# Kernel optimization log

Hardware: AMD Instinct MI355X
Metric: run time of the kernel (lower is better)

## Reference

```python
import jax, jax.numpy as jnp
import numpy as np

B, N, P, K, C = 8, 4096, 4096, 32, 128  # batch, points, npoint, neighbors, channels (=mlp[-1])
W_OUT = 16  # weightnet output channels (from Linear(16*mlp[-1], mlp[-1]))
EPS = 1e-5


def setup_inputs() -> dict:
    key = jax.random.key(0)
    ks = jax.random.split(key, 9)
    xyz = jax.random.normal(ks[0], (B, P, 3), jnp.float32)
    points = jax.random.normal(ks[1], (B, N, C), jnp.float32)
    local_coordinates = jax.random.normal(ks[2], (B, P, K, 3), jnp.float32)
    neighbor_lists = jax.random.randint(ks[3], (B, P, K), 0, N)
    data_idx = jax.random.randint(ks[4], (B,), 0, B)
    Ww = jax.random.normal(ks[5], (3, W_OUT), jnp.float32) * 0.1   # weightnet (pointwise linear 3->16)
    bw = jnp.zeros((W_OUT,), jnp.float32)
    Wl = jax.random.normal(ks[6], (W_OUT * C, C), jnp.float32) * 0.02  # nn.Linear(16*mlp[-1], mlp[-1])
    bl = jnp.zeros((C,), jnp.float32)
    gamma = jnp.ones((C,), jnp.float32)   # BatchNorm1d weight
    beta = jnp.zeros((C,), jnp.float32)   # BatchNorm1d bias
    return {"xyz": xyz, "points": points, "local_coordinates": local_coordinates,
            "neighbor_lists": neighbor_lists, "data_idx": data_idx,
            "Ww": Ww, "bw": bw, "Wl": Wl, "bl": bl, "gamma": gamma, "beta": beta}


def reference(xyz, points, local_coordinates, neighbor_lists, data_idx, Ww, bw, Wl, bl, gamma, beta):
    b, p, k, _ = local_coordinates.shape
    c = points.shape[-1]
    # weightnet: pointwise map of 3-D local coordinates to 16 weight channels -> [B,P,K,16]
    weights = local_coordinates @ Ww + bw
    # irregular neighbor gather: data[b,p,k,:] = points[b, neighbor_lists[b,p,k], :] -> [B,P,K,C]
    data = points[jnp.arange(b)[:, None, None], neighbor_lists]
    # per-point weighted aggregation over K neighbors: [B,P,C,16] -> flatten to [B,P,C*16]
    new_points = jnp.einsum('bpkc,bpkw->bpcw', data, weights).reshape(b, p, c * weights.shape[-1])
    # batch reindex via data_idx
    new_points = new_points[data_idx]
    # linear tail: [B,P,C]
    new_points = new_points @ Wl + bl
    # BatchNorm1d over channel dim (training-mode batch stats), then ReLU: [B,C,P]
    x = new_points.transpose(0, 2, 1)
    mean = x.mean(axis=(0, 2), keepdims=True)
    var = x.var(axis=(0, 2), keepdims=True)
    x = (x - mean) * jax.lax.rsqrt(var + EPS) * gamma[None, :, None] + beta[None, :, None]
    return xyz, jax.nn.relu(x)
```

## Files before the change

### kernel.cpp

```cpp
#include <hip/hip_runtime.h>

#define Bn 8
#define Nn 4096
#define Pn 4096
#define Kn 32
#define Cn 128

using float4v = __attribute__((ext_vector_type(4))) float;
using short8  = __attribute__((ext_vector_type(8))) short;

__device__ __forceinline__ unsigned short bf16b(float f) {
  union { float f; unsigned u; } v; v.f = f;
  unsigned r = v.u + 0x7FFFu + ((v.u >> 16) & 1u);
  return (unsigned short)(r >> 16);
}

__device__ __forceinline__ unsigned pkhi(float x, float y) {
  return __builtin_amdgcn_perm(__float_as_uint(y), __float_as_uint(x), 0x07060302u);
}

__global__ __launch_bounds__(256) void prep(const float* __restrict__ Wl,
                                            unsigned short* __restrict__ WlT,
                                            const float* __restrict__ xyz,
                                            float* __restrict__ out,
                                            float* __restrict__ gacc) {
  __shared__ unsigned short tile[128 * 33];
  const int t = threadIdx.x, blk = blockIdx.x;
  if (blk < 64) {
#pragma unroll
    for (int i = 0; i < 16; ++i) {
      int idx = i * 256 + t;
      int kl = idx >> 7, n = idx & 127;
      tile[n * 33 + kl] = bf16b(Wl[(size_t)(blk * 32 + kl) * 128 + n]);
    }
    __syncthreads();
#pragma unroll
    for (int i = 0; i < 16; ++i) {
      int idx = i * 256 + t;
      int n = idx >> 5, kl = idx & 31;
      WlT[(size_t)n * 2048 + blk * 32 + kl] = tile[n * 33 + kl];
    }
  } else {
    if (blk == 64) gacc[t] = 0.f;
    const int i0 = (blk - 64) * 3072 + t * 12;
#pragma unroll
    for (int i = 0; i < 3; ++i)
      *(float4v*)(out + i0 + i * 4) = *(const float4v*)(xyz + i0 + i * 4);
  }
}

__global__ __launch_bounds__(256, 4) void fused(
    const float* __restrict__ points, const float* __restrict__ lc,
    const int* __restrict__ nl, const int* __restrict__ didx,
    const float* __restrict__ Ww, const float* __restrict__ bwv,
    const unsigned short* __restrict__ WlT, const float* __restrict__ blv,
    float* __restrict__ xout, float* __restrict__ gacc) {
  __shared__ unsigned short Mlds[32 * 256 + 7424];
  __shared__ int nlds[32 * 32];
  __shared__ float red[256];

  const int t = threadIdx.x, lane = t & 63, w = t >> 6;
  const int l15 = lane & 15, q = lane >> 4;
  const int b = blockIdx.x & 7;
  const int pg = blockIdx.x >> 3;
  const int p0 = pg * 32;
  const int db = didx[b];
  const char* __restrict__ pbase = (const char*)(points + (size_t)db * Nn * Cn);

  if (blockIdx.x == 0xFFFFFFFFu) ((volatile unsigned short*)Mlds)[32 * 256 + t] = 0;

  {
    int4 nv = *(const int4*)(nl + (size_t)(db * Pn + p0) * Kn + t * 4);
    nv.x <<= 9; nv.y <<= 9; nv.z <<= 9; nv.w <<= 9;
    *(int4*)&nlds[t * 4] = nv;
  }

  const float Ww0 = Ww[l15], Ww1 = Ww[16 + l15], Ww2 = Ww[32 + l15];
  const float bw0 = bwv[l15];

  short8 af[8];
#pragma unroll
  for (int i = 0; i < 8; ++i) {
    const int p = p0 + w * 8 + i;
    const int pk = (db * Pn + p) * Kn;
    const float* __restrict__ lcp = lc + (size_t)(pk + q * 8) * 3;
    float la[24];
#pragma unroll
    for (int v = 0; v < 6; ++v) *(float4v*)&la[v * 4] = *(const float4v*)(lcp + v * 4);
#pragma unroll
    for (int j = 0; j < 8; ++j) {
      float ww = bw0 + la[3 * j] * Ww0 + la[3 * j + 1] * Ww1 + la[3 * j + 2] * Ww2;
      af[i][j] = (short)bf16b(ww);
    }
  }

  float4v acc[2][2];
#pragma unroll
  for (int pt = 0; pt < 2; ++pt)
#pragma unroll
    for (int nt = 0; nt < 2; ++nt) acc[pt][nt] = (float4v){0.f, 0.f, 0.f, 0.f};

  __syncthreads();

  const unsigned short* __restrict__ bpt =
      WlT + (size_t)(w * 32 + l15) * 2048 + q * 8;
  const unsigned cvoff = (unsigned)(l15 * 4);

#define ISSUE(i, ct, fdst)                                                 \
  {                                                                        \
    const int pi_ = w * 8 + (i);                                           \
    int nk_[8];                                                            \
    *(int4*)&nk_[0] = *(const int4*)&nlds[pi_ * 32 + q * 8];               \
    *(int4*)&nk_[4] = *(const int4*)&nlds[pi_ * 32 + q * 8 + 4];           \
    _Pragma("unroll") for (int j = 0; j < 8; ++j)                          \
        fdst[j] = *(const float*)(pbase + ((unsigned)nk_[j] + cvoff +      \
                                           (unsigned)((ct) * 64)));        \
  }

#define FIN(i, fsrc)                                                       \
  {                                                                        \
    const int pi_ = w * 8 + (i);                                           \
    union { short8 s; unsigned u[4]; } bv_;                                \
    bv_.u[0] = pkhi(fsrc[0], fsrc[1]);                                     \
    bv_.u[1] = pkhi(fsrc[2], fsrc[3]);                                     \
    bv_.u[2] = pkhi(fsrc[4], fsrc[5]);                                     \
    bv_.u[3] = pkhi(fsrc[6], fsrc[7]);                                     \
    float4v d_ = {0.f, 0.f, 0.f, 0.f};                                     \
    d_ = __builtin_amdgcn_mfma_f32_16x16x32_bf16(af[i], bv_.s, d_, 0, 0, 0); \
    const unsigned off_ = (unsigned)(pi_ * 512 + ((l15 * 32 + q * 8) ^     \
        ((((pi_ & 7) ^ (l15 & 7)) & 7) << 4)));                            \
    uint2 u_;                                                              \
    u_.x = pkhi(d_[0], d_[1]);                                             \
    u_.y = pkhi(d_[2], d_[3]);                                             \
    *(uint2*)((char*)Mlds + off_) = u_;                                    \
  }

  float fb[4][8];

  for (int ct = 0; ct < 8; ++ct) {
    ISSUE(0, ct, fb[0])
    ISSUE(1, ct, fb[1])
    ISSUE(2, ct, fb[2])
    ISSUE(3, ct, fb[3])
#pragma unroll
    for (int i = 0; i < 8; ++i) {
      FIN(i, fb[i & 3])
      if (i + 4 < 8) ISSUE(i + 4, ct, fb[i & 3])
    }
    __syncthreads();
    const unsigned short* __restrict__ bp = bpt + ct * 256;
    __builtin_amdgcn_s_setprio(1);
#pragma unroll
    for (int ks = 0; ks < 8; ++ks) {
      const unsigned ax = (unsigned)((ks * 64 + q * 16) ^
          ((((l15 & 7) ^ ((ks * 2 + (q >> 1)) & 7)) & 7) << 4));
      short8 a0 = *(const short8*)((const char*)Mlds + l15 * 512 + ax);
      short8 a1 = *(const short8*)((const char*)Mlds + (16 + l15) * 512 + ax);
      short8 b0 = *(const short8*)(bp + ks * 32);
      short8 b1 = *(const short8*)(bp + 32768 + ks * 32);
      acc[0][0] = __builtin_amdgcn_mfma_f32_16x16x32_bf16(a0, b0, acc[0][0], 0, 0, 0);
      acc[0][1] = __builtin_amdgcn_mfma_f32_16x16x32_bf16(a0, b1, acc[0][1], 0, 0, 0);
      acc[1][0] = __builtin_amdgcn_mfma_f32_16x16x32_bf16(a1, b0, acc[1][0], 0, 0, 0);
      acc[1][1] = __builtin_amdgcn_mfma_f32_16x16x32_bf16(a1, b1, acc[1][1], 0, 0, 0);
    }
    __builtin_amdgcn_s_setprio(0);
    __syncthreads();
  }
#undef ISSUE
#undef FIN

#pragma unroll
  for (int nt = 0; nt < 2; ++nt) {
    const int ch = w * 32 + nt * 16 + l15;
    const float bb = blv[ch];
    float s = 0.f, sq = 0.f;
#pragma unroll
    for (int pt = 0; pt < 2; ++pt) {
      float4v o;
#pragma unroll
      for (int r = 0; r < 4; ++r) {
        float v = acc[pt][nt][r] + bb; o[r] = v; s += v; sq += v * v;
      }
      *(float4v*)(xout + ((size_t)(b * Cn + ch)) * Pn + p0 + pt * 16 + q * 4) = o;
    }
    s += __shfl_xor(s, 16); s += __shfl_xor(s, 32);
    sq += __shfl_xor(sq, 16); sq += __shfl_xor(sq, 32);
    if (lane < 16) { red[ch] = s; red[128 + ch] = sq; }
  }
  __syncthreads();
  atomicAdd(&gacc[t], red[t]);
}

__global__ __launch_bounds__(256) void finalize_ln(float* __restrict__ x,
                                                   const float* __restrict__ gacc,
                                                   const float* __restrict__ gamma,
                                                   const float* __restrict__ beta) {
  const int idx = blockIdx.x * 256 + threadIdx.x;
  const int fi = idx * 4;
  const int c = (fi >> 12) & 127;
  const float inv = 1.f / 32768.f;
  const float mean = gacc[c] * inv;
  const float var = gacc[128 + c] * inv - mean * mean;
  const float scale = rsqrtf(var + 1e-5f) * gamma[c];
  const float shift = beta[c] - mean * scale;
  float4v v = *(float4v*)(x + fi);
#pragma unroll
  for (int r = 0; r < 4; ++r) v[r] = fmaxf(v[r] * scale + shift, 0.f);
  *(float4v*)(x + fi) = v;
}

extern "C" void kernel_launch(void* const* d_in, const int* in_sizes, int n_in,
                              void* d_out, int out_size, void* d_ws, size_t ws_size,
                              hipStream_t stream) {
  const float* xyz    = (const float*)d_in[0];
  const float* points = (const float*)d_in[1];
  const float* lc     = (const float*)d_in[2];
  const int*   nl     = (const int*)d_in[3];
  const int*   didx   = (const int*)d_in[4];
  const float* Ww     = (const float*)d_in[5];
  const float* bw     = (const float*)d_in[6];
  const float* Wl     = (const float*)d_in[7];
  const float* bl     = (const float*)d_in[8];
  const float* gamma  = (const float*)d_in[9];
  const float* beta   = (const float*)d_in[10];

  float* out  = (float*)d_out;
  float* xout = out + (size_t)Bn * Pn * 3;
  unsigned short* WlT = (unsigned short*)d_ws;
  float* gacc = (float*)((char*)d_ws + (size_t)512 * 1024);

  prep<<<96, 256, 0, stream>>>(Wl, WlT, xyz, out, gacc);
  fused<<<1024, 256, 0, stream>>>(points, lc, nl, didx, Ww, bw, WlT, bl,
                                  xout, gacc);
  finalize_ln<<<4096, 256, 0, stream>>>(xout, gacc, gamma, beta);
}
```

Measured before the change: 191.6 us.

## Gather neighbor features via global_load_lds into double-buffered LDS slabs

Replaces the register-based gather of neighbor features with direct global-to-LDS loads (global_load_lds) into a per-wave double-buffered slab, synchronised with explicit vmcnt waits and sched barriers. This frees registers and keeps gathers in flight while the weightnet MFMA and bf16 packing run. It also software-prefetches the WlT B-operand one k-step ahead in the tail GEMM loop and removes the LDS padding dummy. The code depends on the hand-written vmcnt counts being exact and adds LDS reads back to registers.

Result: slower. 196.5 us (+2.5%).

```diff
diff --git a/kernel.cpp b/kernel.cpp
--- a/kernel.cpp
+++ b/kernel.cpp
@@ -55,7 +55,8 @@
     const float* __restrict__ Ww, const float* __restrict__ bwv,
     const unsigned short* __restrict__ WlT, const float* __restrict__ blv,
     float* __restrict__ xout, float* __restrict__ gacc) {
-  __shared__ unsigned short Mlds[32 * 256 + 7424];
+  __shared__ float slab[4][2][512];
+  __shared__ unsigned short Mlds[32 * 256];
   __shared__ int nlds[32 * 32];
   __shared__ float red[256];
 
@@ -67,8 +68,6 @@
   const int db = didx[b];
   const char* __restrict__ pbase = (const char*)(points + (size_t)db * Nn * Cn);
 
-  if (blockIdx.x == 0xFFFFFFFFu) ((volatile unsigned short*)Mlds)[32 * 256 + t] = 0;
-
   {
     int4 nv = *(const int4*)(nl + (size_t)(db * Pn + p0) * Kn + t * 4);
     nv.x <<= 9; nv.y <<= 9; nv.z <<= 9; nv.w <<= 9;
@@ -106,15 +105,22 @@
       WlT + (size_t)(w * 32 + l15) * 2048 + q * 8;
   const unsigned cvoff = (unsigned)(l15 * 4);
 
-#define ISSUE(i, ct, fdst)                                                 \
+#define WAITV8 asm volatile("s_waitcnt vmcnt(8)" ::: "memory")
+#define WAITV0 asm volatile("s_waitcnt vmcnt(0)" ::: "memory")
+
+#define DMA(i, ct, bsel)                                                   \
   {                                                                        \
     const int pi_ = w * 8 + (i);                                           \
     int nk_[8];                                                            \
     *(int4*)&nk_[0] = *(const int4*)&nlds[pi_ * 32 + q * 8];               \
     *(int4*)&nk_[4] = *(const int4*)&nlds[pi_ * 32 + q * 8 + 4];           \
     _Pragma("unroll") for (int j = 0; j < 8; ++j)                          \
-        fdst[j] = *(const float*)(pbase + ((unsigned)nk_[j] + cvoff +      \
-                                           (unsigned)((ct) * 64)));        \
+        __builtin_amdgcn_global_load_lds(                                  \
+            (const __attribute__((address_space(1))) unsigned int*)        \
+                (pbase + ((unsigned)nk_[j] + cvoff + (unsigned)((ct) * 64))), \
+            (__attribute__((address_space(3))) unsigned int*)              \
+                (&slab[w][bsel][(j) * 64]),                                \
+            4, 0, 0);                                                      \
   }
 
 #define FIN(i, fsrc)                                                       \
@@ -135,39 +141,52 @@
     *(uint2*)((char*)Mlds + off_) = u_;                                    \
   }
 
-  float fb[4][8];
-
   for (int ct = 0; ct < 8; ++ct) {
-    ISSUE(0, ct, fb[0])
-    ISSUE(1, ct, fb[1])
-    ISSUE(2, ct, fb[2])
-    ISSUE(3, ct, fb[3])
+    DMA(0, ct, 0)
+    DMA(1, ct, 1)
 #pragma unroll
     for (int i = 0; i < 8; ++i) {
-      FIN(i, fb[i & 3])
-      if (i + 4 < 8) ISSUE(i + 4, ct, fb[i & 3])
+      if (i < 7) { WAITV8; } else { WAITV0; }
+      __builtin_amdgcn_sched_barrier(0);
+      float f[8];
+      const float* ls = &slab[w][i & 1][(unsigned)(q * 16 + l15)];
+#pragma unroll
+      for (int j = 0; j < 8; ++j) f[j] = ls[j * 64];
+      FIN(i, f)
+      if (i < 6) {
+        __builtin_amdgcn_sched_barrier(0);
+        DMA(i + 2, ct, i & 1)
+      }
     }
     __syncthreads();
     const unsigned short* __restrict__ bp = bpt + ct * 256;
+    short8 b0A = *(const short8*)(bp);
+    short8 b1A = *(const short8*)(bp + 32768);
     __builtin_amdgcn_s_setprio(1);
 #pragma unroll
     for (int ks = 0; ks < 8; ++ks) {
+      short8 b0B, b1B;
+      if (ks < 7) {
+        b0B = *(const short8*)(bp + (ks + 1) * 32);
+        b1B = *(const short8*)(bp + 32768 + (ks + 1) * 32);
+      }
       const unsigned ax = (unsigned)((ks * 64 + q * 16) ^
           ((((l15 & 7) ^ ((ks * 2 + (q >> 1)) & 7)) & 7) << 4));
       short8 a0 = *(const short8*)((const char*)Mlds + l15 * 512 + ax);
       short8 a1 = *(const short8*)((const char*)Mlds + (16 + l15) * 512 + ax);
-      short8 b0 = *(const short8*)(bp + ks * 32);
-      short8 b1 = *(const short8*)(bp + 32768 + ks * 32);
-      acc[0][0] = __builtin_amdgcn_mfma_f32_16x16x32_bf16(a0, b0, acc[0][0], 0, 0, 0);
-      acc[0][1] = __builtin_amdgcn_mfma_f32_16x16x32_bf16(a0, b1, acc[0][1], 0, 0, 0);
-      acc[1][0] = __builtin_amdgcn_mfma_f32_16x16x32_bf16(a1, b0, acc[1][0], 0, 0, 0);
-      acc[1][1] = __builtin_amdgcn_mfma_f32_16x16x32_bf16(a1, b1, acc[1][1], 0, 0, 0);
+      acc[0][0] = __builtin_amdgcn_mfma_f32_16x16x32_bf16(a0, b0A, acc[0][0], 0, 0, 0);
+      acc[0][1] = __builtin_amdgcn_mfma_f32_16x16x32_bf16(a0, b1A, acc[0][1], 0, 0, 0);
+      acc[1][0] = __builtin_amdgcn_mfma_f32_16x16x32_bf16(a1, b0A, acc[1][0], 0, 0, 0);
+      acc[1][1] = __builtin_amdgcn_mfma_f32_16x16x32_bf16(a1, b1A, acc[1][1], 0, 0, 0);
+      b0A = b0B; b1A = b1B;
     }
     __builtin_amdgcn_s_setprio(0);
     __syncthreads();
   }
-#undef ISSUE
+#undef DMA
 #undef FIN
+#undef WAITV8
+#undef WAITV0
 
 #pragma unroll
   for (int nt = 0; nt < 2; ++nt) {
```

## Fuse prep, main and batchnorm kernels into one kernel with grid barriers

Applied to the files above, without the earlier changes.

Merges the weight-transpose prep, the gather/MFMA kernel and the batchnorm finalize into a single launch. Atomic counters let blocks wait for the transposed weights, and a grid-wide barrier lets every block apply normalization and ReLU to its accumulators still held in registers. This avoids writing the pre-norm output and then reading and rewriting it, and removes two kernel launches. In exchange it adds a memset, spin-wait barriers, and relies on all 1024 blocks being resident at once; if they are not, the kernel deadlocks.

Result: slower. 499.4 us (+160.6%).

```diff
diff --git a/kernel.cpp b/kernel.cpp
--- a/kernel.cpp
+++ b/kernel.cpp
@@ -19,13 +19,36 @@
   return __builtin_amdgcn_perm(__float_as_uint(y), __float_as_uint(x), 0x07060302u);
 }
 
-__global__ __launch_bounds__(256) void prep(const float* __restrict__ Wl,
-                                            unsigned short* __restrict__ WlT,
-                                            const float* __restrict__ xyz,
-                                            float* __restrict__ out,
-                                            float* __restrict__ gacc) {
+__global__ __launch_bounds__(256, 4) void mega(
+    const float* __restrict__ points, const float* __restrict__ lc,
+    const int* __restrict__ nl, const int* __restrict__ didx,
+    const float* __restrict__ Ww, const float* __restrict__ bwv,
+    const float* __restrict__ Wl, const float* __restrict__ blv,
+    const float* __restrict__ gamma, const float* __restrict__ beta,
+    const float* __restrict__ xyz, float* __restrict__ out,
+    unsigned short* __restrict__ WlT, float* __restrict__ gacc,
+    unsigned* __restrict__ ctrs) {
+  __shared__ unsigned short Mlds[32 * 256];
+  __shared__ int nlds[32 * 32];
+  __shared__ float red[256];
   __shared__ unsigned short tile[128 * 33];
-  const int t = threadIdx.x, blk = blockIdx.x;
+
+  const int t = threadIdx.x, lane = t & 63, w = t >> 6;
+  const int l15 = lane & 15, q = lane >> 4;
+  const int blk = blockIdx.x;
+  const int b = blk & 7;
+  const int pg = blk >> 3;
+  const int p0 = pg * 32;
+  const int db = didx[b];
+  const char* __restrict__ pbase = (const char*)(points + (size_t)db * Nn * Cn);
+  float* __restrict__ xout = out + (size_t)Bn * Pn * 3;
+
+  {
+    int4 nv = *(const int4*)(nl + (size_t)(db * Pn + p0) * Kn + t * 4);
+    nv.x <<= 9; nv.y <<= 9; nv.z <<= 9; nv.w <<= 9;
+    *(int4*)&nlds[t * 4] = nv;
+  }
+
   if (blk < 64) {
 #pragma unroll
     for (int i = 0; i < 16; ++i) {
@@ -40,39 +63,15 @@
       int n = idx >> 5, kl = idx & 31;
       WlT[(size_t)n * 2048 + blk * 32 + kl] = tile[n * 33 + kl];
     }
-  } else {
-    if (blk == 64) gacc[t] = 0.f;
+    __syncthreads();
+    if (t == 0)
+      __hip_atomic_fetch_add(&ctrs[0], 1u, __ATOMIC_RELEASE,
+                             __HIP_MEMORY_SCOPE_AGENT);
+  } else if (blk < 96) {
     const int i0 = (blk - 64) * 3072 + t * 12;
 #pragma unroll
     for (int i = 0; i < 3; ++i)
       *(float4v*)(out + i0 + i * 4) = *(const float4v*)(xyz + i0 + i * 4);
-  }
-}
-
-__global__ __launch_bounds__(256, 4) void fused(
-    const float* __restrict__ points, const float* __restrict__ lc,
-    const int* __restrict__ nl, const int* __restrict__ didx,
-    const float* __restrict__ Ww, const float* __restrict__ bwv,
-    const unsigned short* __restrict__ WlT, const float* __restrict__ blv,
-    float* __restrict__ xout, float* __restrict__ gacc) {
-  __shared__ unsigned short Mlds[32 * 256 + 7424];
-  __shared__ int nlds[32 * 32];
-  __shared__ float red[256];
-
-  const int t = threadIdx.x, lane = t & 63, w = t >> 6;
-  const int l15 = lane & 15, q = lane >> 4;
-  const int b = blockIdx.x & 7;
-  const int pg = blockIdx.x >> 3;
-  const int p0 = pg * 32;
-  const int db = didx[b];
-  const char* __restrict__ pbase = (const char*)(points + (size_t)db * Nn * Cn);
-
-  if (blockIdx.x == 0xFFFFFFFFu) ((volatile unsigned short*)Mlds)[32 * 256 + t] = 0;
-
-  {
-    int4 nv = *(const int4*)(nl + (size_t)(db * Pn + p0) * Kn + t * 4);
-    nv.x <<= 9; nv.y <<= 9; nv.z <<= 9; nv.w <<= 9;
-    *(int4*)&nlds[t * 4] = nv;
   }
 
   const float Ww0 = Ww[l15], Ww1 = Ww[16 + l15], Ww2 = Ww[32 + l15];
@@ -148,6 +147,14 @@
       if (i + 4 < 8) ISSUE(i + 4, ct, fb[i & 3])
     }
     __syncthreads();
+    if (ct == 0) {
+      if (t == 0) {
+        while (__hip_atomic_load(&ctrs[0], __ATOMIC_ACQUIRE,
+                                 __HIP_MEMORY_SCOPE_AGENT) < 64u)
+          __builtin_amdgcn_s_sleep(2);
+      }
+      __syncthreads();
+    }
     const unsigned short* __restrict__ bp = bpt + ct * 256;
     __builtin_amdgcn_s_setprio(1);
 #pragma unroll
@@ -175,38 +182,50 @@
     const float bb = blv[ch];
     float s = 0.f, sq = 0.f;
 #pragma unroll
-    for (int pt = 0; pt < 2; ++pt) {
-      float4v o;
+    for (int pt = 0; pt < 2; ++pt)
 #pragma unroll
       for (int r = 0; r < 4; ++r) {
-        float v = acc[pt][nt][r] + bb; o[r] = v; s += v; sq += v * v;
+        float v = acc[pt][nt][r] + bb; s += v; sq += v * v;
       }
-      *(float4v*)(xout + ((size_t)(b * Cn + ch)) * Pn + p0 + pt * 16 + q * 4) = o;
-    }
     s += __shfl_xor(s, 16); s += __shfl_xor(s, 32);
     sq += __shfl_xor(sq, 16); sq += __shfl_xor(sq, 32);
     if (lane < 16) { red[ch] = s; red[128 + ch] = sq; }
   }
   __syncthreads();
   atomicAdd(&gacc[t], red[t]);
-}
-
-__global__ __launch_bounds__(256) void finalize_ln(float* __restrict__ x,
-                                                   const float* __restrict__ gacc,
-                                                   const float* __restrict__ gamma,
-                                                   const float* __restrict__ beta) {
-  const int idx = blockIdx.x * 256 + threadIdx.x;
-  const int fi = idx * 4;
-  const int c = (fi >> 12) & 127;
+  __syncthreads();
+  if (t == 0)
+    __hip_atomic_fetch_add(&ctrs[1], 1u, __ATOMIC_RELEASE,
+                           __HIP_MEMORY_SCOPE_AGENT);
+  if (t == 0) {
+    while (__hip_atomic_load(&ctrs[1], __ATOMIC_ACQUIRE,
+                             __HIP_MEMORY_SCOPE_AGENT) < 1024u)
+      __builtin_amdgcn_s_sleep(4);
+  }
+  __syncthreads();
+
   const float inv = 1.f / 32768.f;
-  const float mean = gacc[c] * inv;
-  const float var = gacc[128 + c] * inv - mean * mean;
-  const float scale = rsqrtf(var + 1e-5f) * gamma[c];
-  const float shift = beta[c] - mean * scale;
-  float4v v = *(float4v*)(x + fi);
-#pragma unroll
-  for (int r = 0; r < 4; ++r) v[r] = fmaxf(v[r] * scale + shift, 0.f);
-  *(float4v*)(x + fi) = v;
+#pragma unroll
+  for (int nt = 0; nt < 2; ++nt) {
+    const int ch = w * 32 + nt * 16 + l15;
+    const float bb = blv[ch];
+    const float g1 = __hip_atomic_load(&gacc[ch], __ATOMIC_RELAXED,
+                                       __HIP_MEMORY_SCOPE_AGENT);
+    const float g2 = __hip_atomic_load(&gacc[128 + ch], __ATOMIC_RELAXED,
+                                       __HIP_MEMORY_SCOPE_AGENT);
+    const float mean = g1 * inv;
+    const float var = g2 * inv - mean * mean;
+    const float scale = rsqrtf(var + 1e-5f) * gamma[ch];
+    const float shift = beta[ch] - mean * scale;
+#pragma unroll
+    for (int pt = 0; pt < 2; ++pt) {
+      float4v o;
+#pragma unroll
+      for (int r = 0; r < 4; ++r)
+        o[r] = fmaxf((acc[pt][nt][r] + bb) * scale + shift, 0.f);
+      *(float4v*)(xout + ((size_t)(b * Cn + ch)) * Pn + p0 + pt * 16 + q * 4) = o;
+    }
+  }
 }
 
 extern "C" void kernel_launch(void* const* d_in, const int* in_sizes, int n_in,
@@ -225,12 +244,11 @@
   const float* beta   = (const float*)d_in[10];
 
   float* out  = (float*)d_out;
-  float* xout = out + (size_t)Bn * Pn * 3;
   unsigned short* WlT = (unsigned short*)d_ws;
   float* gacc = (float*)((char*)d_ws + (size_t)512 * 1024);
-
-  prep<<<96, 256, 0, stream>>>(Wl, WlT, xyz, out, gacc);
-  fused<<<1024, 256, 0, stream>>>(points, lc, nl, didx, Ww, bw, WlT, bl,
-                                  xout, gacc);
-  finalize_ln<<<4096, 256, 0, stream>>>(xout, gacc, gamma, beta);
-}
+  unsigned* ctrs = (unsigned*)((char*)d_ws + (size_t)512 * 1024 + 1024);
+
+  hipMemsetAsync((char*)d_ws + (size_t)512 * 1024, 0, 1024 + 64, stream);
+  mega<<<1024, 256, 0, stream>>>(points, lc, nl, didx, Ww, bw, Wl, bl,
+                                 gamma, beta, xyz, out, WlT, gacc, ctrs);
+}
```

## Fold prep kernel into fused kernel with atomic flag handoff for WlT

Applied to the files above, without the earlier changes.

The separate prep kernel, which transposes Wl to bf16 WlT and copies xyz, is merged into the first blocks of the fused kernel. Other blocks spin on a global atomic counter before their first MFMA stage that reads WlT, and a memset replaces the in-kernel zeroing of gacc. This removes one kernel launch and its serialization gap but adds a spin-wait dependency. The scheme assumes the first 64 blocks get scheduled, which holds with 1024 blocks at occupancy 4.

Result: slower. 197.4 us (+3.0%).

```diff
diff --git a/kernel.cpp b/kernel.cpp
--- a/kernel.cpp
+++ b/kernel.cpp
@@ -19,13 +19,35 @@
   return __builtin_amdgcn_perm(__float_as_uint(y), __float_as_uint(x), 0x07060302u);
 }
 
-__global__ __launch_bounds__(256) void prep(const float* __restrict__ Wl,
-                                            unsigned short* __restrict__ WlT,
-                                            const float* __restrict__ xyz,
-                                            float* __restrict__ out,
-                                            float* __restrict__ gacc) {
+__global__ __launch_bounds__(256, 4) void fused(
+    const float* __restrict__ points, const float* __restrict__ lc,
+    const int* __restrict__ nl, const int* __restrict__ didx,
+    const float* __restrict__ Ww, const float* __restrict__ bwv,
+    const float* __restrict__ Wl, const float* __restrict__ blv,
+    const float* __restrict__ xyz, float* __restrict__ out,
+    unsigned short* __restrict__ WlT, float* __restrict__ gacc,
+    unsigned* __restrict__ ctrs) {
+  __shared__ unsigned short Mlds[32 * 256];
   __shared__ unsigned short tile[128 * 33];
-  const int t = threadIdx.x, blk = blockIdx.x;
+  __shared__ int nlds[32 * 32];
+  __shared__ float red[256];
+
+  const int t = threadIdx.x, lane = t & 63, w = t >> 6;
+  const int l15 = lane & 15, q = lane >> 4;
+  const int blk = blockIdx.x;
+  const int b = blk & 7;
+  const int pg = blk >> 3;
+  const int p0 = pg * 32;
+  const int db = didx[b];
+  const char* __restrict__ pbase = (const char*)(points + (size_t)db * Nn * Cn);
+  float* __restrict__ xout = out + (size_t)Bn * Pn * 3;
+
+  {
+    int4 nv = *(const int4*)(nl + (size_t)(db * Pn + p0) * Kn + t * 4);
+    nv.x <<= 9; nv.y <<= 9; nv.z <<= 9; nv.w <<= 9;
+    *(int4*)&nlds[t * 4] = nv;
+  }
+
   if (blk < 64) {
 #pragma unroll
     for (int i = 0; i < 16; ++i) {
@@ -40,39 +62,15 @@
       int n = idx >> 5, kl = idx & 31;
       WlT[(size_t)n * 2048 + blk * 32 + kl] = tile[n * 33 + kl];
     }
-  } else {
-    if (blk == 64) gacc[t] = 0.f;
+    __syncthreads();
+    if (t == 0)
+      __hip_atomic_fetch_add(&ctrs[0], 1u, __ATOMIC_RELEASE,
+                             __HIP_MEMORY_SCOPE_AGENT);
+  } else if (blk < 96) {
     const int i0 = (blk - 64) * 3072 + t * 12;
 #pragma unroll
     for (int i = 0; i < 3; ++i)
       *(float4v*)(out + i0 + i * 4) = *(const float4v*)(xyz + i0 + i * 4);
-  }
-}
-
-__global__ __launch_bounds__(256, 4) void fused(
-    const float* __restrict__ points, const float* __restrict__ lc,
-    const int* __restrict__ nl, const int* __restrict__ didx,
-    const float* __restrict__ Ww, const float* __restrict__ bwv,
-    const unsigned short* __restrict__ WlT, const float* __restrict__ blv,
-    float* __restrict__ xout, float* __restrict__ gacc) {
-  __shared__ unsigned short Mlds[32 * 256 + 7424];
-  __shared__ int nlds[32 * 32];
-  __shared__ float red[256];
-
-  const int t = threadIdx.x, lane = t & 63, w = t >> 6;
-  const int l15 = lane & 15, q = lane >> 4;
-  const int b = blockIdx.x & 7;
-  const int pg = blockIdx.x >> 3;
-  const int p0 = pg * 32;
-  const int db = didx[b];
-  const char* __restrict__ pbase = (const char*)(points + (size_t)db * Nn * Cn);
-
-  if (blockIdx.x == 0xFFFFFFFFu) ((volatile unsigned short*)Mlds)[32 * 256 + t] = 0;
-
-  {
-    int4 nv = *(const int4*)(nl + (size_t)(db * Pn + p0) * Kn + t * 4);
-    nv.x <<= 9; nv.y <<= 9; nv.z <<= 9; nv.w <<= 9;
-    *(int4*)&nlds[t * 4] = nv;
   }
 
   const float Ww0 = Ww[l15], Ww1 = Ww[16 + l15], Ww2 = Ww[32 + l15];
@@ -148,6 +146,14 @@
       if (i + 4 < 8) ISSUE(i + 4, ct, fb[i & 3])
     }
     __syncthreads();
+    if (ct == 0) {
+      if (t == 0) {
+        while (__hip_atomic_load(&ctrs[0], __ATOMIC_ACQUIRE,
+                                 __HIP_MEMORY_SCOPE_AGENT) < 64u)
+          __builtin_amdgcn_s_sleep(4);
+      }
+      __syncthreads();
+    }
     const unsigned short* __restrict__ bp = bpt + ct * 256;
     __builtin_amdgcn_s_setprio(1);
 #pragma unroll
@@ -228,9 +234,10 @@
   float* xout = out + (size_t)Bn * Pn * 3;
   unsigned short* WlT = (unsigned short*)d_ws;
   float* gacc = (float*)((char*)d_ws + (size_t)512 * 1024);
-
-  prep<<<96, 256, 0, stream>>>(Wl, WlT, xyz, out, gacc);
-  fused<<<1024, 256, 0, stream>>>(points, lc, nl, didx, Ww, bw, WlT, bl,
-                                  xout, gacc);
+  unsigned* ctrs = (unsigned*)((char*)d_ws + (size_t)512 * 1024 + 1024);
+
+  hipMemsetAsync((char*)d_ws + (size_t)512 * 1024, 0, 1024 + 64, stream);
+  fused<<<1024, 256, 0, stream>>>(points, lc, nl, didx, Ww, bw, Wl, bl,
+                                  xyz, out, WlT, gacc, ctrs);
   finalize_ln<<<4096, 256, 0, stream>>>(xout, gacc, gamma, beta);
 }
```
